# Performance work log

Hardware: AMD Instinct MI355X
Metric: run time of the kernel (lower is better)

## Reference

```python
import jax, jax.numpy as jnp
import numpy as np

BATCH, IN_DIM, OUT_DIM = 8192, 4096, 4096
BASE_LR = 0.015
PRED_ERR = 0.0


def setup_inputs() -> dict:
    key = jax.random.key(0)
    ks = jax.random.split(key, 6)
    x = jax.random.normal(ks[0], (BATCH, IN_DIM), jnp.float32)
    # W_slow ~ orthogonal init with gain 1.4 (approximated by scaled gaussian)
    W_slow = jax.random.normal(ks[1], (OUT_DIM, IN_DIM), jnp.float32) * (1.4 / np.sqrt(IN_DIM))
    W_fast = jax.random.normal(ks[2], (OUT_DIM, IN_DIM), jnp.float32) * 0.01
    gamma = jnp.ones((OUT_DIM,), jnp.float32)
    beta = jnp.zeros((OUT_DIM,), jnp.float32)
    w1 = jax.random.normal(ks[3], (16, 2), jnp.float32) * 0.5
    b1 = jnp.zeros((16,), jnp.float32)
    w2 = jax.random.normal(ks[4], (1, 16), jnp.float32) * 0.5
    b2 = jnp.full((1,), -2.0, jnp.float32)  # plasticity_controller[2].bias = -2.0
    global_plasticity = jnp.float32(0.5)
    return {"x": x, "W_slow": W_slow, "W_fast": W_fast, "gamma": gamma,
            "beta": beta, "w1": w1, "b1": b1, "w2": w2, "b2": b2,
            "global_plasticity": global_plasticity}


def reference(x, W_slow, W_fast, gamma, beta, w1, b1, w2, b2, global_plasticity):
    # dual linear sum: slow + fast pathway, [B, out_dim]
    pre_act = x @ W_slow.T + x @ W_fast.T

    # per-output-column batch stats (torch std is unbiased, ddof=1)
    batch_mean = pre_act.mean(axis=0)                       # [out_dim]
    batch_std = pre_act.std(axis=0, ddof=1) + 1e-6          # [out_dim]
    stats = jnp.stack([batch_mean, batch_std], axis=1)      # [out_dim, 2]

    # tiny 2-16-1 plasticity controller MLP
    h = jnp.tanh(stats @ w1.T + b1)                          # [out_dim, 16]
    learned_plasticity = jax.nn.sigmoid(h @ w2.T + b2)[:, 0] # [out_dim]
    eff = global_plasticity * learned_plasticity * (1.0 - PRED_ERR)

    # LayerNorm (eps=1e-5) + soft-clipped tanh output
    mu = pre_act.mean(axis=-1, keepdims=True)
    var = pre_act.var(axis=-1, keepdims=True)
    ln = (pre_act - mu) * jax.lax.rsqrt(var + 1e-5) * gamma + beta
    out = 5.0 * jnp.tanh(ln / 5.0)

    # Hebbian fast-weight update (training branch), functional version
    B = x.shape[0]
    x_norm = (x ** 2).sum(axis=1).mean() + 1e-6
    correlation = (out.T @ x) / B                            # [out_dim, in_dim]
    forgetting = 0.2 * W_fast
    delta = jnp.clip(correlation / x_norm - forgetting, -0.05, 0.05)
    lr_vector = eff[:, None] * BASE_LR
    W_fast_updated = (W_fast + delta * lr_vector) * 0.999
    new_W_fast = jnp.where(eff.mean() > 0.001, W_fast_updated, W_fast)

    return out, new_W_fast
```

## Files before the change

### kernel.cpp

```cpp
#include <hip/hip_runtime.h>
#include <stdint.h>

#define B_DIM 8192
#define K_DIM 4096
#define N_DIM 4096

typedef unsigned short u16;
typedef float f4 __attribute__((ext_vector_type(4)));
typedef float f32x4 __attribute__((ext_vector_type(4)));
typedef __bf16 bf16x8 __attribute__((ext_vector_type(8)));
typedef unsigned short u16x8 __attribute__((ext_vector_type(8)));
typedef unsigned short u16x4 __attribute__((ext_vector_type(4)));

#define AS1(p) ((const __attribute__((address_space(1))) void*)(p))
#define AS3(p) ((__attribute__((address_space(3))) void*)(p))

__device__ __forceinline__ u16 f2bf(float f) {
  uint32_t u = __builtin_bit_cast(uint32_t, f);
  u += 0x7fffu + ((u >> 16) & 1u);
  return (u16)(u >> 16);
}

__device__ __forceinline__ float wred(float v) {
#pragma unroll
  for (int o = 32; o > 0; o >>= 1) v += __shfl_xor(v, o);
  return v;
}

__global__ void k_init(float* __restrict__ stats) {
  for (int i = threadIdx.x; i < 8194; i += 256) stats[i] = 0.0f;
}

__global__ __launch_bounds__(256) void k_prep_w(const f4* __restrict__ wslow, const f4* __restrict__ wfast,
                                                u16x4* __restrict__ wo) {
  size_t stride = (size_t)gridDim.x * 256;
  size_t n4 = (size_t)N_DIM * K_DIM / 4;
  for (size_t i = (size_t)blockIdx.x * 256 + threadIdx.x; i < n4; i += stride) {
    f4 a = wslow[i], b = wfast[i];
    u16x4 o;
#pragma unroll
    for (int j = 0; j < 4; ++j) o[j] = f2bf(a[j] + b[j]);
    wo[i] = o;
  }
}

__global__ __launch_bounds__(256) void k_prep_xT(const float* __restrict__ x, u16* __restrict__ xb,
                                                 u16* __restrict__ xT, float* __restrict__ xsumsq) {
  __shared__ u16 tile[64][68];
  __shared__ float red[4];
  int tk = blockIdx.x, tb = blockIdx.y;
  int t = threadIdx.x;
  float s = 0.f;
#pragma unroll
  for (int q = 0; q < 4; ++q) {
    int idx = q * 256 + t;
    int row = idx >> 4, cg = idx & 15;
    f4 v = *(const f4*)&x[(size_t)(tb * 64 + row) * K_DIM + tk * 64 + cg * 4];
    u16x4 o;
#pragma unroll
    for (int j = 0; j < 4; ++j) { o[j] = f2bf(v[j]); s += v[j] * v[j]; }
    *(u16x4*)&xb[(size_t)(tb * 64 + row) * K_DIM + tk * 64 + cg * 4] = o;
    *(u16x4*)&tile[row][cg * 4] = o;
  }
  s = wred(s);
  if ((t & 63) == 0) red[t >> 6] = s;
  __syncthreads();
  if (t == 0) atomicAdd(xsumsq, red[0] + red[1] + red[2] + red[3]);
#pragma unroll
  for (int q = 0; q < 2; ++q) {
    int idx = q * 256 + t;
    int row = idx >> 3, cg = idx & 7;
    u16x8 v;
#pragma unroll
    for (int j = 0; j < 8; ++j) v[j] = tile[cg * 8 + j][row];
    *(u16x8*)&xT[(size_t)(tk * 64 + row) * B_DIM + tb * 64 + cg * 8] = v;
  }
}

__global__ __launch_bounds__(512, 2) void gemm8(const u16* __restrict__ A, const u16* __restrict__ Bm,
                                                float* __restrict__ C, int M, int N, int K,
                                                float* __restrict__ colsum, float* __restrict__ colsumsq,
                                                const float* __restrict__ wfast, const float* __restrict__ eff,
                                                const float* __restrict__ sc) {
  __shared__ __align__(16) u16 As[32768];
  __shared__ __align__(16) u16 Bs[32768];

  const int tid = threadIdx.x, wave = tid >> 6, lane = tid & 63;
  const int li = lane & 15, hi = lane >> 4;
  const int wm = wave >> 2, wn = wave & 3;

  const int GX = N >> 8;
  const int nwg = GX * (M >> 8);
  int bid = blockIdx.y * GX + blockIdx.x;
  int swz = (bid & 7) * (nwg >> 3) + (bid >> 3);
  const int bx = swz % GX, by = swz / GX;
  const int m0 = by * 256, n0 = bx * 256;

  int srcoff[2][2];
#pragma unroll
  for (int h = 0; h < 2; ++h)
#pragma unroll
    for (int q = 0; q < 2; ++q) {
      int O = h * 16384 + q * 8192 + wave * 1024 + lane * 16;
      int T = O ^ (((O >> 7) & 7) << 4);
      srcoff[h][q] = (T >> 7) * K + ((T & 127) >> 1);
    }

  const u16* Abase = A + (size_t)m0 * K;
  const u16* Bbase = Bm + (size_t)n0 * K;

#define STG_A(buf, h, kt) do { \
  __builtin_amdgcn_global_load_lds(AS1(Abase + (kt) + srcoff[h][0]), AS3(&As[(buf)*16384 + (h)*8192 + wave*512]), 16, 0, 0); \
  __builtin_amdgcn_global_load_lds(AS1(Abase + (kt) + srcoff[h][1]), AS3(&As[(buf)*16384 + (h)*8192 + 4096 + wave*512]), 16, 0, 0); \
} while (0)
#define STG_B(buf, h, kt) do { \
  __builtin_amdgcn_global_load_lds(AS1(Bbase + (kt) + srcoff[h][0]), AS3(&Bs[(buf)*16384 + (h)*8192 + wave*512]), 16, 0, 0); \
  __builtin_amdgcn_global_load_lds(AS1(Bbase + (kt) + srcoff[h][1]), AS3(&Bs[(buf)*16384 + (h)*8192 + 4096 + wave*512]), 16, 0, 0); \
} while (0)

  const int xa = (li & 7) << 3;
  const int abase = (wm * 128 + li) * 64 + hi * 8;
  const int bbase = (wn * 64 + li) * 64 + hi * 8;
#define LDA_(dst, buf, m, ks) dst = *(const bf16x8*)&As[(buf)*16384 + (((abase + (m)*1024 + (ks)*32)) ^ xa)]
#define LDB_(dst, buf, n, ks) dst = *(const bf16x8*)&Bs[(buf)*16384 + (((bbase + (n)*1024 + (ks)*32)) ^ xa)]

  f32x4 acc[8][4] = {};
  bf16x8 a[8][2], b[4][2];
  const int NT = K >> 6;

  STG_A(0, 0, 0); STG_A(0, 1, 0); STG_B(0, 0, 0); STG_B(0, 1, 0);
  STG_A(1, 0, 64); STG_A(1, 1, 64); STG_B(1, 0, 64);
  asm volatile("s_waitcnt vmcnt(6)" ::: "memory");
  __builtin_amdgcn_s_barrier();

  for (int t = 0; t < NT; ++t) {
    const int buf = t & 1;
    const int ktn = (t + 1) << 6, ktnn = (t + 2) << 6;

#pragma unroll
    for (int m = 0; m < 4; ++m) { LDA_(a[m][0], buf, m, 0); LDA_(a[m][1], buf, m, 1); }
#pragma unroll
    for (int n = 0; n < 2; ++n) { LDB_(b[n][0], buf, n, 0); LDB_(b[n][1], buf, n, 1); }
    if (t + 1 < NT) STG_B(buf ^ 1, 1, ktn);
    __builtin_amdgcn_s_barrier();
    asm volatile("s_waitcnt lgkmcnt(0)" ::: "memory");
    __builtin_amdgcn_sched_barrier(0);
    __builtin_amdgcn_s_setprio(1);
#pragma unroll
    for (int ks = 0; ks < 2; ++ks)
#pragma unroll
      for (int m = 0; m < 4; ++m)
#pragma unroll
        for (int n = 0; n < 2; ++n)
          acc[m][n] = __builtin_amdgcn_mfma_f32_16x16x32_bf16(a[m][ks], b[n][ks], acc[m][n], 0, 0, 0);
    __builtin_amdgcn_s_setprio(0);
    __builtin_amdgcn_s_barrier();

#pragma unroll
    for (int m = 4; m < 8; ++m) { LDA_(a[m][0], buf, m, 0); LDA_(a[m][1], buf, m, 1); }
    __builtin_amdgcn_s_barrier();
    asm volatile("s_waitcnt lgkmcnt(0)" ::: "memory");
    __builtin_amdgcn_sched_barrier(0);
    __builtin_amdgcn_s_setprio(1);
#pragma unroll
    for (int ks = 0; ks < 2; ++ks)
#pragma unroll
      for (int m = 4; m < 8; ++m)
#pragma unroll
        for (int n = 0; n < 2; ++n)
          acc[m][n] = __builtin_amdgcn_mfma_f32_16x16x32_bf16(a[m][ks], b[n][ks], acc[m][n], 0, 0, 0);
    __builtin_amdgcn_s_setprio(0);
    __builtin_amdgcn_s_barrier();

#pragma unroll
    for (int n = 2; n < 4; ++n) { LDB_(b[n][0], buf, n, 0); LDB_(b[n][1], buf, n, 1); }
    if (t + 2 < NT) { STG_A(buf, 0, ktnn); STG_A(buf, 1, ktnn); }
    __builtin_amdgcn_s_barrier();
    asm volatile("s_waitcnt lgkmcnt(0)" ::: "memory");
    __builtin_amdgcn_sched_barrier(0);
    __builtin_amdgcn_s_setprio(1);
#pragma unroll
    for (int ks = 0; ks < 2; ++ks)
#pragma unroll
      for (int m = 0; m < 4; ++m)
#pragma unroll
        for (int n = 2; n < 4; ++n)
          acc[m][n] = __builtin_amdgcn_mfma_f32_16x16x32_bf16(a[m][ks], b[n][ks], acc[m][n], 0, 0, 0);
    __builtin_amdgcn_s_setprio(0);
    __builtin_amdgcn_s_barrier();

    if (t + 2 < NT) STG_B(buf, 0, ktnn);
    __builtin_amdgcn_s_barrier();
    __builtin_amdgcn_s_setprio(1);
#pragma unroll
    for (int ks = 0; ks < 2; ++ks)
#pragma unroll
      for (int m = 4; m < 8; ++m)
#pragma unroll
        for (int n = 2; n < 4; ++n)
          acc[m][n] = __builtin_amdgcn_mfma_f32_16x16x32_bf16(a[m][ks], b[n][ks], acc[m][n], 0, 0, 0);
    __builtin_amdgcn_s_setprio(0);
    if (t + 1 < NT) {
      if (t + 2 < NT) asm volatile("s_waitcnt vmcnt(6)" ::: "memory");
      else            asm volatile("s_waitcnt vmcnt(0)" ::: "memory");
    }
    __builtin_amdgcn_s_barrier();
  }

  if (wfast) {
    float xn = sc[0] * (1.0f / 8192.0f) + 1e-6f;
    float inv = 1.0f / (8192.0f * xn);
    bool on = (sc[1] * (1.0f / 4096.0f)) > 0.001f;
    const int colb = n0 + wn * 64 + li;
    const int rowb = m0 + wm * 128 + hi * 4;
#pragma unroll
    for (int m = 0; m < 8; ++m) {
      f4 e4 = *(const f4*)&eff[rowb + m * 16];
#pragma unroll
      for (int j = 0; j < 4; ++j) {
        float lr = e4[j] * 0.015f;
        const size_t ro = (size_t)(rowb + m * 16 + j) * N;
#pragma unroll
        for (int n = 0; n < 4; ++n) {
          float w = wfast[ro + colb + n * 16];
          float delta = fminf(fmaxf(acc[m][n][j] * inv - 0.2f * w, -0.05f), 0.05f);
          C[ro + colb + n * 16] = on ? (w + delta * lr) * 0.999f : w;
        }
      }
    }
  } else {
    float* Cp = C + (size_t)(m0 + wm * 128 + hi * 4) * N + n0 + wn * 64 + li;
#pragma unroll
    for (int m = 0; m < 8; ++m)
#pragma unroll
      for (int n = 0; n < 4; ++n)
#pragma unroll
        for (int j = 0; j < 4; ++j)
          Cp[(size_t)(m * 16 + j) * N + n * 16] = acc[m][n][j];
    if (colsum) {
#pragma unroll
      for (int n = 0; n < 4; ++n) {
        float s = 0.f, q = 0.f;
#pragma unroll
        for (int m = 0; m < 8; ++m)
#pragma unroll
          for (int j = 0; j < 4; ++j) { float v = acc[m][n][j]; s += v; q += v * v; }
        s += __shfl_xor(s, 16); s += __shfl_xor(s, 32);
        q += __shfl_xor(q, 16); q += __shfl_xor(q, 32);
        if (hi == 0) {
          int col = n0 + wn * 64 + n * 16 + li;
          atomicAdd(&colsum[col], s);
          atomicAdd(&colsumsq[col], q);
        }
      }
    }
  }
#undef STG_A
#undef STG_B
#undef LDA_
#undef LDB_
}

__global__ __launch_bounds__(256) void k_mlp(const float* __restrict__ colsum, const float* __restrict__ colsumsq,
                                             const float* __restrict__ w1, const float* __restrict__ b1,
                                             const float* __restrict__ w2, const float* __restrict__ b2,
                                             const float* __restrict__ gp, float* __restrict__ eff,
                                             float* __restrict__ effsum) {
  __shared__ float red[4];
  int c = blockIdx.x * 256 + threadIdx.x;
  float mean = colsum[c] * (1.0f / B_DIM);
  float var = (colsumsq[c] - (float)B_DIM * mean * mean) * (1.0f / (B_DIM - 1));
  float sd = sqrtf(fmaxf(var, 0.f)) + 1e-6f;
  float acc = b2[0];
#pragma unroll
  for (int i = 0; i < 16; ++i) {
    float h = tanhf(mean * w1[2 * i] + sd * w1[2 * i + 1] + b1[i]);
    acc += h * w2[i];
  }
  float p = 1.0f / (1.0f + expf(-acc));
  float e = gp[0] * p;
  eff[c] = e;
  float s = wred(e);
  int lane = threadIdx.x & 63, wave = threadIdx.x >> 6;
  if (lane == 0) red[wave] = s;
  __syncthreads();
  if (threadIdx.x == 0) atomicAdd(effsum, red[0] + red[1] + red[2] + red[3]);
}

__global__ __launch_bounds__(256) void k_ln(const float* __restrict__ pre, const float* __restrict__ gamma,
                                            const float* __restrict__ beta, float* __restrict__ outF,
                                            u16* __restrict__ outB) {
  __shared__ float row[N_DIM];
  __shared__ float red[2][4];
  int t = threadIdx.x, lane = t & 63, wave = t >> 6;
  const float* p = pre + (size_t)blockIdx.x * N_DIM;
  float s = 0.f;
#pragma unroll
  for (int q = 0; q < 4; ++q) {
    int c = (q * 256 + t) * 4;
    f4 v = *(const f4*)&p[c];
    *(f4*)&row[c] = v;
    s += v[0] + v[1] + v[2] + v[3];
  }
  s = wred(s);
  if (lane == 0) red[0][wave] = s;
  __syncthreads();
  float mean = (red[0][0] + red[0][1] + red[0][2] + red[0][3]) * (1.0f / N_DIM);
  float vs = 0.f;
#pragma unroll
  for (int q = 0; q < 4; ++q) {
    int c = (q * 256 + t) * 4;
    f4 v = *(const f4*)&row[c];
#pragma unroll
    for (int j = 0; j < 4; ++j) { float d = v[j] - mean; vs += d * d; }
  }
  vs = wred(vs);
  if (lane == 0) red[1][wave] = vs;
  __syncthreads();
  float var = (red[1][0] + red[1][1] + red[1][2] + red[1][3]) * (1.0f / N_DIM);
  float rstd = rsqrtf(var + 1e-5f);
  float* o = outF + (size_t)blockIdx.x * N_DIM;
  u16* ob = outB + (size_t)blockIdx.x * N_DIM;
#pragma unroll
  for (int q = 0; q < 4; ++q) {
    int c = (q * 256 + t) * 4;
    f4 v = *(const f4*)&row[c];
    f4 g = *(const f4*)&gamma[c];
    f4 be = *(const f4*)&beta[c];
    f4 r;
    u16x4 rb;
#pragma unroll
    for (int j = 0; j < 4; ++j) {
      float ln = (v[j] - mean) * rstd * g[j] + be[j];
      float ov = 5.0f * tanhf(ln * 0.2f);
      r[j] = ov; rb[j] = f2bf(ov);
    }
    *(f4*)&o[c] = r;
    *(u16x4*)&ob[c] = rb;
  }
}

__global__ __launch_bounds__(256) void k_transpose(const u16* __restrict__ src, u16* __restrict__ dst,
                                                   int R, int C) {
  __shared__ u16 tile[64][65];
  int tc = blockIdx.x, tr = blockIdx.y;
  int t = threadIdx.x;
#pragma unroll
  for (int q = 0; q < 2; ++q) {
    int idx = q * 256 + t;
    int row = idx >> 3, cg = idx & 7;
    u16x8 v = *(const u16x8*)&src[(size_t)(tr * 64 + row) * C + tc * 64 + cg * 8];
#pragma unroll
    for (int j = 0; j < 8; ++j) tile[row][cg * 8 + j] = v[j];
  }
  __syncthreads();
#pragma unroll
  for (int q = 0; q < 2; ++q) {
    int idx = q * 256 + t;
    int row = idx >> 3, cg = idx & 7;
    u16x8 v;
#pragma unroll
    for (int j = 0; j < 8; ++j) v[j] = tile[cg * 8 + j][row];
    *(u16x8*)&dst[(size_t)(tc * 64 + row) * R + tr * 64 + cg * 8] = v;
  }
}

extern "C" void kernel_launch(void* const* d_in, const int* in_sizes, int n_in,
                              void* d_out, int out_size, void* d_ws, size_t ws_size,
                              hipStream_t stream) {
  const float* x      = (const float*)d_in[0];
  const float* W_slow = (const float*)d_in[1];
  const float* W_fast = (const float*)d_in[2];
  const float* gamma  = (const float*)d_in[3];
  const float* beta   = (const float*)d_in[4];
  const float* w1     = (const float*)d_in[5];
  const float* b1     = (const float*)d_in[6];
  const float* w2     = (const float*)d_in[7];
  const float* b2     = (const float*)d_in[8];
  const float* gp     = (const float*)d_in[9];

  float* outF = (float*)d_out;
  float* outW = (float*)d_out + (size_t)B_DIM * N_DIM;

  uint8_t* ws = (uint8_t*)d_ws;
  u16*  x_bf   = (u16*)(ws + 0);
  u16*  outT   = (u16*)(ws + 0);
  u16*  wsum   = (u16*)(ws + 67108864);
  u16*  out_bf = (u16*)(ws + 67108864);
  u16*  xT     = (u16*)(ws + 134217728);
  float* stats = (float*)(ws + 201326592);
  float* colsum   = stats;
  float* colsumsq = stats + 4096;
  float* xsumsq   = stats + 8192;
  float* effsum   = stats + 8193;
  float* eff      = stats + 8448;

  k_init<<<1, 256, 0, stream>>>(stats);
  k_prep_w<<<2048, 256, 0, stream>>>((const f4*)W_slow, (const f4*)W_fast, (u16x4*)wsum);
  k_prep_xT<<<dim3(K_DIM / 64, B_DIM / 64), 256, 0, stream>>>(x, x_bf, xT, xsumsq);
  gemm8<<<dim3(N_DIM / 256, B_DIM / 256), 512, 0, stream>>>(x_bf, wsum, outF, B_DIM, N_DIM, K_DIM,
                                                            colsum, colsumsq, nullptr, nullptr, nullptr);
  k_mlp<<<N_DIM / 256, 256, 0, stream>>>(colsum, colsumsq, w1, b1, w2, b2, gp, eff, effsum);
  k_ln<<<B_DIM, 256, 0, stream>>>(outF, gamma, beta, outF, out_bf);
  k_transpose<<<dim3(N_DIM / 64, B_DIM / 64), 256, 0, stream>>>(out_bf, outT, B_DIM, N_DIM);
  gemm8<<<dim3(K_DIM / 256, N_DIM / 256), 512, 0, stream>>>(outT, xT, outW, N_DIM, K_DIM, B_DIM,
                                                            nullptr, nullptr, W_fast, eff, xsumsq);
}
```

Measured before the change: 758.3 us.

## Restructure GEMM inner loop by k-halves to cut registers, fold init into prep

The GEMM main loop now runs its four MFMA phases over k-slices (ks=0 then ks=1) with full 4x4 n coverage, instead of splitting the n dimension. This halves the A/B fragment registers (a[4], b[4] instead of a[8][2], b[4][2]) and reorders the global-to-LDS staging so that A quarter-tiles and both B halves are issued at different points. The stats-zeroing kernel is folded into the weight-prep kernel to remove one launch. The new staging order changes when buffers are overwritten and needs correct barrier and vmcnt accounting. The added LDS reads per phase could also shift the balance between memory and MFMA work.

```diff
diff --git a/kernel.cpp b/kernel.cpp
--- a/kernel.cpp
+++ b/kernel.cpp
@@ -27,12 +27,10 @@
   return v;
 }
 
-__global__ void k_init(float* __restrict__ stats) {
-  for (int i = threadIdx.x; i < 8194; i += 256) stats[i] = 0.0f;
-}
-
 __global__ __launch_bounds__(256) void k_prep_w(const f4* __restrict__ wslow, const f4* __restrict__ wfast,
-                                                u16x4* __restrict__ wo) {
+                                                u16x4* __restrict__ wo, float* __restrict__ stats) {
+  if (blockIdx.x == 0)
+    for (int i = threadIdx.x; i < 8194; i += 256) stats[i] = 0.0f;
   size_t stride = (size_t)gridDim.x * 256;
   size_t n4 = (size_t)N_DIM * K_DIM / 4;
   for (size_t i = (size_t)blockIdx.x * 256 + threadIdx.x; i < n4; i += stride) {
@@ -109,9 +107,9 @@
   const u16* Abase = A + (size_t)m0 * K;
   const u16* Bbase = Bm + (size_t)n0 * K;
 
-#define STG_A(buf, h, kt) do { \
-  __builtin_amdgcn_global_load_lds(AS1(Abase + (kt) + srcoff[h][0]), AS3(&As[(buf)*16384 + (h)*8192 + wave*512]), 16, 0, 0); \
-  __builtin_amdgcn_global_load_lds(AS1(Abase + (kt) + srcoff[h][1]), AS3(&As[(buf)*16384 + (h)*8192 + 4096 + wave*512]), 16, 0, 0); \
+#define STG_AQ(buf, sub, kt) do { \
+  __builtin_amdgcn_global_load_lds(AS1(Abase + (kt) + srcoff[0][sub]), AS3(&As[(buf)*16384 + (sub)*4096 + wave*512]), 16, 0, 0); \
+  __builtin_amdgcn_global_load_lds(AS1(Abase + (kt) + srcoff[1][sub]), AS3(&As[(buf)*16384 + 8192 + (sub)*4096 + wave*512]), 16, 0, 0); \
 } while (0)
 #define STG_B(buf, h, kt) do { \
   __builtin_amdgcn_global_load_lds(AS1(Bbase + (kt) + srcoff[h][0]), AS3(&Bs[(buf)*16384 + (h)*8192 + wave*512]), 16, 0, 0); \
@@ -125,11 +123,11 @@
 #define LDB_(dst, buf, n, ks) dst = *(const bf16x8*)&Bs[(buf)*16384 + (((bbase + (n)*1024 + (ks)*32)) ^ xa)]
 
   f32x4 acc[8][4] = {};
-  bf16x8 a[8][2], b[4][2];
+  bf16x8 a[4], b[4];
   const int NT = K >> 6;
 
-  STG_A(0, 0, 0); STG_A(0, 1, 0); STG_B(0, 0, 0); STG_B(0, 1, 0);
-  STG_A(1, 0, 64); STG_A(1, 1, 64); STG_B(1, 0, 64);
+  STG_AQ(0, 0, 0); STG_AQ(0, 1, 0); STG_B(0, 0, 0); STG_B(0, 1, 0);
+  STG_AQ(1, 0, 64); STG_B(1, 0, 64); STG_B(1, 1, 64);
   asm volatile("s_waitcnt vmcnt(6)" ::: "memory");
   __builtin_amdgcn_s_barrier();
 
@@ -138,67 +136,64 @@
     const int ktn = (t + 1) << 6, ktnn = (t + 2) << 6;
 
 #pragma unroll
-    for (int m = 0; m < 4; ++m) { LDA_(a[m][0], buf, m, 0); LDA_(a[m][1], buf, m, 1); }
-#pragma unroll
-    for (int n = 0; n < 2; ++n) { LDB_(b[n][0], buf, n, 0); LDB_(b[n][1], buf, n, 1); }
-    if (t + 1 < NT) STG_B(buf ^ 1, 1, ktn);
+    for (int m = 0; m < 4; ++m) LDA_(a[m], buf, m, 0);
+#pragma unroll
+    for (int n = 0; n < 4; ++n) LDB_(b[n], buf, n, 0);
+    if (t + 1 < NT) STG_AQ(buf ^ 1, 1, ktn);
     __builtin_amdgcn_s_barrier();
     asm volatile("s_waitcnt lgkmcnt(0)" ::: "memory");
     __builtin_amdgcn_sched_barrier(0);
     __builtin_amdgcn_s_setprio(1);
 #pragma unroll
-    for (int ks = 0; ks < 2; ++ks)
-#pragma unroll
-      for (int m = 0; m < 4; ++m)
-#pragma unroll
-        for (int n = 0; n < 2; ++n)
-          acc[m][n] = __builtin_amdgcn_mfma_f32_16x16x32_bf16(a[m][ks], b[n][ks], acc[m][n], 0, 0, 0);
+    for (int m = 0; m < 4; ++m)
+#pragma unroll
+      for (int n = 0; n < 4; ++n)
+        acc[m][n] = __builtin_amdgcn_mfma_f32_16x16x32_bf16(a[m], b[n], acc[m][n], 0, 0, 0);
     __builtin_amdgcn_s_setprio(0);
     __builtin_amdgcn_s_barrier();
 
 #pragma unroll
-    for (int m = 4; m < 8; ++m) { LDA_(a[m][0], buf, m, 0); LDA_(a[m][1], buf, m, 1); }
+    for (int m = 0; m < 4; ++m) LDA_(a[m], buf, m + 4, 0);
     __builtin_amdgcn_s_barrier();
     asm volatile("s_waitcnt lgkmcnt(0)" ::: "memory");
     __builtin_amdgcn_sched_barrier(0);
     __builtin_amdgcn_s_setprio(1);
 #pragma unroll
-    for (int ks = 0; ks < 2; ++ks)
-#pragma unroll
-      for (int m = 4; m < 8; ++m)
-#pragma unroll
-        for (int n = 0; n < 2; ++n)
-          acc[m][n] = __builtin_amdgcn_mfma_f32_16x16x32_bf16(a[m][ks], b[n][ks], acc[m][n], 0, 0, 0);
+    for (int m = 0; m < 4; ++m)
+#pragma unroll
+      for (int n = 0; n < 4; ++n)
+        acc[m + 4][n] = __builtin_amdgcn_mfma_f32_16x16x32_bf16(a[m], b[n], acc[m + 4][n], 0, 0, 0);
     __builtin_amdgcn_s_setprio(0);
     __builtin_amdgcn_s_barrier();
 
 #pragma unroll
-    for (int n = 2; n < 4; ++n) { LDB_(b[n][0], buf, n, 0); LDB_(b[n][1], buf, n, 1); }
-    if (t + 2 < NT) { STG_A(buf, 0, ktnn); STG_A(buf, 1, ktnn); }
+    for (int m = 0; m < 4; ++m) LDA_(a[m], buf, m, 1);
+#pragma unroll
+    for (int n = 0; n < 4; ++n) LDB_(b[n], buf, n, 1);
     __builtin_amdgcn_s_barrier();
     asm volatile("s_waitcnt lgkmcnt(0)" ::: "memory");
     __builtin_amdgcn_sched_barrier(0);
     __builtin_amdgcn_s_setprio(1);
 #pragma unroll
-    for (int ks = 0; ks < 2; ++ks)
-#pragma unroll
-      for (int m = 0; m < 4; ++m)
-#pragma unroll
-        for (int n = 2; n < 4; ++n)
-          acc[m][n] = __builtin_amdgcn_mfma_f32_16x16x32_bf16(a[m][ks], b[n][ks], acc[m][n], 0, 0, 0);
+    for (int m = 0; m < 4; ++m)
+#pragma unroll
+      for (int n = 0; n < 4; ++n)
+        acc[m][n] = __builtin_amdgcn_mfma_f32_16x16x32_bf16(a[m], b[n], acc[m][n], 0, 0, 0);
     __builtin_amdgcn_s_setprio(0);
     __builtin_amdgcn_s_barrier();
 
-    if (t + 2 < NT) STG_B(buf, 0, ktnn);
-    __builtin_amdgcn_s_barrier();
+#pragma unroll
+    for (int m = 0; m < 4; ++m) LDA_(a[m], buf, m + 4, 1);
+    if (t + 2 < NT) { STG_AQ(buf, 0, ktnn); STG_B(buf, 0, ktnn); STG_B(buf, 1, ktnn); }
+    __builtin_amdgcn_s_barrier();
+    asm volatile("s_waitcnt lgkmcnt(0)" ::: "memory");
+    __builtin_amdgcn_sched_barrier(0);
     __builtin_amdgcn_s_setprio(1);
 #pragma unroll
-    for (int ks = 0; ks < 2; ++ks)
-#pragma unroll
-      for (int m = 4; m < 8; ++m)
-#pragma unroll
-        for (int n = 2; n < 4; ++n)
-          acc[m][n] = __builtin_amdgcn_mfma_f32_16x16x32_bf16(a[m][ks], b[n][ks], acc[m][n], 0, 0, 0);
+    for (int m = 0; m < 4; ++m)
+#pragma unroll
+      for (int n = 0; n < 4; ++n)
+        acc[m + 4][n] = __builtin_amdgcn_mfma_f32_16x16x32_bf16(a[m], b[n], acc[m + 4][n], 0, 0, 0);
     __builtin_amdgcn_s_setprio(0);
     if (t + 1 < NT) {
       if (t + 2 < NT) asm volatile("s_waitcnt vmcnt(6)" ::: "memory");
@@ -255,7 +250,7 @@
       }
     }
   }
-#undef STG_A
+#undef STG_AQ
 #undef STG_B
 #undef LDA_
 #undef LDB_
@@ -395,8 +390,7 @@
   float* effsum   = stats + 8193;
   float* eff      = stats + 8448;
 
-  k_init<<<1, 256, 0, stream>>>(stats);
-  k_prep_w<<<2048, 256, 0, stream>>>((const f4*)W_slow, (const f4*)W_fast, (u16x4*)wsum);
+  k_prep_w<<<2048, 256, 0, stream>>>((const f4*)W_slow, (const f4*)W_fast, (u16x4*)wsum, stats);
   k_prep_xT<<<dim3(K_DIM / 64, B_DIM / 64), 256, 0, stream>>>(x, x_bf, xT, xsumsq);
   gemm8<<<dim3(N_DIM / 256, B_DIM / 256), 512, 0, stream>>>(x_bf, wsum, outF, B_DIM, N_DIM, K_DIM,
                                                             colsum, colsumsq, nullptr, nullptr, nullptr);
```

Measured after the change: 835.9 us. +10.2%, slower.
